# Optimization experiments

Hardware: AMD Instinct MI355X
Metric: run time of the kernel (lower is better)

The kernel has to match this reference:

```python
import jax, jax.numpy as jnp
import numpy as np

GRID = 25
NUM_NODE = GRID * GRID  # 625, hard-coded by the original module

def _neighbor_flat_indices():
    # Replicates the torch index construction exactly, incl. boundary shifts.
    offsets = np.array([[-1,-1],[-1,0],[-1,1],[0,-1],[0,0],[0,1],[1,-1],[1,0],[1,1]])
    idx = np.arange(NUM_NODE)
    rows = idx // GRID
    cols = idx % GRID
    nr = rows[:, None] + offsets[:, 0]   # [625, 9]
    nc = cols[:, None] + offsets[:, 1]
    nr = nr.reshape(GRID, GRID, 9)
    nr[0, :, :] += 1                     # reflect top boundary
    nr[-1, :, :] -= 1                    # reflect bottom boundary
    nr = nr.reshape(NUM_NODE, 9)
    nc = nc.reshape(GRID, GRID, 9)
    nc[:, 0, :] += 1                     # reflect left boundary
    nc[:, -1, :] -= 1                    # reflect right boundary
    nc = nc.reshape(NUM_NODE, 9)
    return jnp.asarray(nr * GRID + nc)   # [625, 9] flat node indices

NEIGH = _neighbor_flat_indices()

def setup_inputs() -> dict:
    key = jax.random.key(0)
    k1, k2, k3, k4, k5 = jax.random.split(key, 5)
    B = 512
    x = jax.random.normal(k1, (B, NUM_NODE, 66), dtype=jnp.float32)
    # nn.Linear(66, 64): weight [64, 66], bias [64]
    W_fc = jax.random.normal(k2, (64, 66), dtype=jnp.float32) * (1.0 / np.sqrt(66))
    b_fc = jax.random.normal(k3, (64,), dtype=jnp.float32) * 0.01
    # nn.Linear(128, 1): weight [1, 128], bias [1]
    W_at = jax.random.normal(k4, (1, 128), dtype=jnp.float32) * (1.0 / np.sqrt(128))
    b_at = jax.random.normal(k5, (1,), dtype=jnp.float32) * 0.01
    return {"x": x, "W_fc": W_fc, "b_fc": b_fc, "W_at": W_at, "b_at": b_at}

def reference(x, W_fc, b_fc, W_at, b_at):
    # h = fc(x): [B, 625, 64]
    h = jnp.einsum('bnf,df->bnd', x, W_fc) + b_fc
    # Gather fixed 9-neighbor features: [B, 625, 9, 64]
    x2 = h[:, NEIGH, :]
    # Center feature broadcast to the 9 neighbor slots: [B, 625, 9, 64]
    x1 = jnp.broadcast_to(h[:, :, None, :], x2.shape)
    z = jnp.concatenate([x1, x2], axis=-1)                  # [B, 625, 9, 128]
    s = jnp.einsum('bnkf,of->bnko', z, W_at) + b_at          # [B, 625, 9, 1]
    s = jax.nn.leaky_relu(s, negative_slope=0.01)[..., 0]    # [B, 625, 9]
    # exp(s) / sum(exp(s)) over the 9 neighbors == softmax(s)
    attn_weight = jax.nn.softmax(s, axis=-1)                 # [B, 625, 9]
    # Original: sum_k h[:, :, None, :] * w[..., None] over k
    # = h * sum_k w  (h does not depend on k); avoids a [B,625,9,64] temp.
    attn_vector = h * jnp.sum(attn_weight, axis=-1, keepdims=True)  # [B, 625, 64]
    return (attn_vector, attn_weight)
```

## Files before the change

### kernel.cpp

```cpp
#include <hip/hip_runtime.h>

#define BATCH 512
#define GRID_N 25
#define NODES 625
#define BN (BATCH * NODES)
#define NTILES (BN / 16)
#define F 66
#define D 64
#define WPB 4
#define TPW 2
#define NT_BLK (WPB * TPW)
#define STAGE_F (NT_BLK * 16 * F)
#define NBLOCKS (NTILES / NT_BLK)

typedef short bf16x8 __attribute__((ext_vector_type(8)));
typedef float f32x4  __attribute__((ext_vector_type(4)));

__device__ __forceinline__ short f2bf(float f) {
    union { float f; unsigned u; } c; c.f = f;
    unsigned r = c.u + 0x7fffu + ((c.u >> 16) & 1u);
    return (short)(r >> 16);
}

typedef const __attribute__((address_space(1))) void gas_void;
typedef __attribute__((address_space(3))) void las_void;
__device__ __forceinline__ void gload_lds16(const float* g, float* l) {
    __builtin_amdgcn_global_load_lds((gas_void*)g, (las_void*)l, 16, 0, 0);
}

__global__ __launch_bounds__(256, 3) void fc_mfma(
    const float* __restrict__ x, const float* __restrict__ Wfc,
    const float* __restrict__ bfc, const float* __restrict__ Wat,
    float* __restrict__ hout, float* __restrict__ u, float* __restrict__ v)
{
    const int tid  = threadIdx.x;
    const int lane = tid & 63;
    const int wid  = tid >> 6;
    const int l15  = lane & 15;
    const int quad = lane >> 4;

    __shared__ float stage[STAGE_F];
    __shared__ float smem[WPB * 1024];

    const size_t base = (size_t)blockIdx.x * STAGE_F;

#pragma unroll
    for (int it = 0; it < 8; ++it)
        gload_lds16(x + base + it * 1024 + tid * 4,
                    stage + it * 1024 + wid * 256);
    if (wid == 0)
        gload_lds16(x + base + 8192 + lane * 4, stage + 8192);

    bf16x8 bfrag[4][3];
#pragma unroll
    for (int t = 0; t < 4; ++t) {
        const float2* wr = (const float2*)Wfc + (t * 16 + l15) * 33;
#pragma unroll
        for (int c = 0; c < 2; ++c) {
            bf16x8 fr;
#pragma unroll
            for (int j2 = 0; j2 < 4; ++j2) {
                const float2 p = wr[c * 16 + quad * 4 + j2];
                fr[j2 * 2]     = f2bf(p.x);
                fr[j2 * 2 + 1] = f2bf(p.y);
            }
            bfrag[t][c] = fr;
        }
        bf16x8 z = {0, 0, 0, 0, 0, 0, 0, 0};
        if (quad == 0) {
            const float2 p = wr[32];
            z[0] = f2bf(p.x); z[1] = f2bf(p.y);
        }
        bfrag[t][2] = z;
    }
    float bft[4], wa1[4], wa2[4];
#pragma unroll
    for (int t = 0; t < 4; ++t) {
        bft[t] = bfc[t * 16 + l15];
        wa1[t] = Wat[t * 16 + l15];
        wa2[t] = Wat[64 + t * 16 + l15];
    }

    __syncthreads();

    float* tbuf = smem + wid * 1024;

#pragma unroll
    for (int t = 0; t < TPW; ++t) {
        const int bn0 = (blockIdx.x * NT_BLK + wid * TPW + t) * 16;

        const int node = (wid * TPW + t) * 16 + l15;
        const float2* rp = (const float2*)stage + node * 33 + quad * 4;
        bf16x8 afrag[3];
#pragma unroll
        for (int c = 0; c < 2; ++c) {
            bf16x8 fr;
#pragma unroll
            for (int j2 = 0; j2 < 4; ++j2) {
                const float2 p = rp[c * 16 + j2];
                fr[j2 * 2]     = f2bf(p.x);
                fr[j2 * 2 + 1] = f2bf(p.y);
            }
            afrag[c] = fr;
        }
        {
            bf16x8 z = {0, 0, 0, 0, 0, 0, 0, 0};
            if (quad == 0) {
                const float2 p = ((const float2*)stage)[node * 33 + 32];
                z[0] = f2bf(p.x); z[1] = f2bf(p.y);
            }
            afrag[2] = z;
        }

        f32x4 acc[4] = {{0,0,0,0},{0,0,0,0},{0,0,0,0},{0,0,0,0}};
#pragma unroll
        for (int nt = 0; nt < 4; ++nt)
#pragma unroll
            for (int c = 0; c < 3; ++c)
                acc[nt] = __builtin_amdgcn_mfma_f32_16x16x32_bf16(afrag[c], bfrag[nt][c], acc[nt], 0, 0, 0);

        float pu[4] = {0, 0, 0, 0}, pv[4] = {0, 0, 0, 0};
#pragma unroll
        for (int nt = 0; nt < 4; ++nt) {
#pragma unroll
            for (int r = 0; r < 4; ++r) {
                const float h = acc[nt][r] + bft[nt];
                tbuf[(quad * 4 + r) * 64 + nt * 16 + l15] = h;
                pu[r] = fmaf(h, wa1[nt], pu[r]);
                pv[r] = fmaf(h, wa2[nt], pv[r]);
            }
        }
#pragma unroll
        for (int off = 8; off > 0; off >>= 1) {
#pragma unroll
            for (int r = 0; r < 4; ++r) {
                pu[r] += __shfl_xor(pu[r], off, 64);
                pv[r] += __shfl_xor(pv[r], off, 64);
            }
        }
        if (l15 == 0) {
#pragma unroll
            for (int r = 0; r < 4; ++r) {
                u[bn0 + quad * 4 + r] = pu[r];
                v[bn0 + quad * 4 + r] = pv[r];
            }
        }
        float4* dst = (float4*)(hout + (size_t)bn0 * D);
        const float4* src = (const float4*)tbuf;
#pragma unroll
        for (int i = 0; i < 4; ++i)
            dst[i * 64 + lane] = src[i * 64 + lane];
    }
}

__global__ __launch_bounds__(256) void attn_kernel(
    const float* __restrict__ u, const float* __restrict__ v,
    const float* __restrict__ bat, float* __restrict__ wout)
{
    __shared__ float sw[256 * 9];
    const int tid  = threadIdx.x;
    const int lane = tid & 63;
    const int wid  = tid >> 6;
    const int bn   = blockIdx.x * 256 + tid;

    const int b   = bn / NODES;
    const int n   = bn - b * NODES;
    const int row = n / GRID_N;
    const int col = n - row * GRID_N;
    const int r0 = row + (row == 0) - (row == GRID_N - 1);
    const int c0 = col + (col == 0) - (col == GRID_N - 1);

    const float* vb = v + b * NODES;
    const float u0 = u[bn] + bat[0];

    float s[9];
#pragma unroll
    for (int k = 0; k < 9; ++k) {
        const int nr = r0 + (k / 3) - 1;
        const int nc = c0 + (k % 3) - 1;
        const float t = u0 + vb[nr * GRID_N + nc];
        s[k] = (t >= 0.0f) ? t : 0.01f * t;
    }
    float m = s[0];
#pragma unroll
    for (int k = 1; k < 9; ++k) m = fmaxf(m, s[k]);
    float sum = 0.0f;
#pragma unroll
    for (int k = 0; k < 9; ++k) { s[k] = __expf(s[k] - m); sum += s[k]; }
    const float inv = 1.0f / sum;

    float* ws = sw + wid * 576;
#pragma unroll
    for (int k = 0; k < 9; ++k) ws[lane * 9 + k] = s[k] * inv;

    float4* dst = (float4*)(wout + (size_t)(blockIdx.x * 256 + wid * 64) * 9);
    const float4* src = (const float4*)ws;
    dst[lane]      = src[lane];
    dst[64 + lane] = src[64 + lane];
    if (lane < 16) dst[128 + lane] = src[128 + lane];
}

extern "C" void kernel_launch(void* const* d_in, const int* in_sizes, int n_in,
                              void* d_out, int out_size, void* d_ws, size_t ws_size,
                              hipStream_t stream)
{
    const float* x   = (const float*)d_in[0];
    const float* Wfc = (const float*)d_in[1];
    const float* bfc = (const float*)d_in[2];
    const float* Wat = (const float*)d_in[3];
    const float* bat = (const float*)d_in[4];

    float* hout = (float*)d_out;
    float* wout = (float*)d_out + (size_t)BN * D;
    float* u = (float*)d_ws;
    float* v = u + BN;

    fc_mfma<<<NBLOCKS, 256, 0, stream>>>(x, Wfc, bfc, Wat, hout, u, v);
    attn_kernel<<<BN / 256, 256, 0, stream>>>(u, v, bat, wout);
}
```

Measured before the change: 177.5 us.

## Make fc kernel persistent over groups with double-buffered per-wave LDS prefetch

Each block now processes five tile groups instead of one, and each wave keeps its own private LDS slice. The next group's x slice is loaded into a second buffer while the current one is computed, with vmcnt waits replacing the block-wide barrier. The LDS transpose buffer for h is dropped, so h is stored straight from MFMA registers with narrower strided writes. This trades fewer blocks, lower occupancy (launch bounds 3 to 2) and less coalesced h stores for overlap of global loads with compute and less launch and sync overhead.

```diff
diff --git a/kernel.cpp b/kernel.cpp
--- a/kernel.cpp
+++ b/kernel.cpp
@@ -9,9 +9,11 @@
 #define D 64
 #define WPB 4
 #define TPW 2
-#define NT_BLK (WPB * TPW)
-#define STAGE_F (NT_BLK * 16 * F)
-#define NBLOCKS (NTILES / NT_BLK)
+#define NT_GRP (WPB * TPW)
+#define GROUP_F (NT_GRP * 16 * F)
+#define WAVE_F (TPW * 16 * F)
+#define G_PER_BLK 5
+#define NBLOCKS_P (NTILES / (NT_GRP * G_PER_BLK))
 
 typedef short bf16x8 __attribute__((ext_vector_type(8)));
 typedef float f32x4  __attribute__((ext_vector_type(4)));
@@ -28,7 +30,7 @@
     __builtin_amdgcn_global_load_lds((gas_void*)g, (las_void*)l, 16, 0, 0);
 }
 
-__global__ __launch_bounds__(256, 3) void fc_mfma(
+__global__ __launch_bounds__(256, 2) void fc_mfma(
     const float* __restrict__ x, const float* __restrict__ Wfc,
     const float* __restrict__ bfc, const float* __restrict__ Wat,
     float* __restrict__ hout, float* __restrict__ u, float* __restrict__ v)
@@ -39,17 +41,19 @@
     const int l15  = lane & 15;
     const int quad = lane >> 4;
 
-    __shared__ float stage[STAGE_F];
-    __shared__ float smem[WPB * 1024];
-
-    const size_t base = (size_t)blockIdx.x * STAGE_F;
-
-#pragma unroll
-    for (int it = 0; it < 8; ++it)
-        gload_lds16(x + base + it * 1024 + tid * 4,
-                    stage + it * 1024 + wid * 256);
-    if (wid == 0)
-        gload_lds16(x + base + 8192 + lane * 4, stage + 8192);
+    __shared__ float stage[2][WPB][WAVE_F];
+
+    const int gbase = blockIdx.x * G_PER_BLK;
+
+    {
+        const float* src = x + (size_t)gbase * GROUP_F + wid * WAVE_F;
+        float* dst = &stage[0][wid][0];
+#pragma unroll
+        for (int r = 0; r < 8; ++r)
+            gload_lds16(src + r * 256 + lane * 4, dst + r * 256);
+        if (lane < 16)
+            gload_lds16(src + 2048 + lane * 4, dst + 2048);
+    }
 
     bf16x8 bfrag[4][3];
 #pragma unroll
@@ -81,75 +85,86 @@
         wa2[t] = Wat[64 + t * 16 + l15];
     }
 
-    __syncthreads();
-
-    float* tbuf = smem + wid * 1024;
-
-#pragma unroll
-    for (int t = 0; t < TPW; ++t) {
-        const int bn0 = (blockIdx.x * NT_BLK + wid * TPW + t) * 16;
-
-        const int node = (wid * TPW + t) * 16 + l15;
-        const float2* rp = (const float2*)stage + node * 33 + quad * 4;
-        bf16x8 afrag[3];
-#pragma unroll
-        for (int c = 0; c < 2; ++c) {
-            bf16x8 fr;
-#pragma unroll
-            for (int j2 = 0; j2 < 4; ++j2) {
-                const float2 p = rp[c * 16 + j2];
-                fr[j2 * 2]     = f2bf(p.x);
-                fr[j2 * 2 + 1] = f2bf(p.y);
-            }
-            afrag[c] = fr;
-        }
-        {
-            bf16x8 z = {0, 0, 0, 0, 0, 0, 0, 0};
-            if (quad == 0) {
-                const float2 p = ((const float2*)stage)[node * 33 + 32];
-                z[0] = f2bf(p.x); z[1] = f2bf(p.y);
-            }
-            afrag[2] = z;
-        }
-
-        f32x4 acc[4] = {{0,0,0,0},{0,0,0,0},{0,0,0,0},{0,0,0,0}};
-#pragma unroll
-        for (int nt = 0; nt < 4; ++nt)
-#pragma unroll
-            for (int c = 0; c < 3; ++c)
-                acc[nt] = __builtin_amdgcn_mfma_f32_16x16x32_bf16(afrag[c], bfrag[nt][c], acc[nt], 0, 0, 0);
-
-        float pu[4] = {0, 0, 0, 0}, pv[4] = {0, 0, 0, 0};
-#pragma unroll
-        for (int nt = 0; nt < 4; ++nt) {
-#pragma unroll
-            for (int r = 0; r < 4; ++r) {
-                const float h = acc[nt][r] + bft[nt];
-                tbuf[(quad * 4 + r) * 64 + nt * 16 + l15] = h;
-                pu[r] = fmaf(h, wa1[nt], pu[r]);
-                pv[r] = fmaf(h, wa2[nt], pv[r]);
-            }
-        }
-#pragma unroll
-        for (int off = 8; off > 0; off >>= 1) {
-#pragma unroll
-            for (int r = 0; r < 4; ++r) {
-                pu[r] += __shfl_xor(pu[r], off, 64);
-                pv[r] += __shfl_xor(pv[r], off, 64);
-            }
-        }
-        if (l15 == 0) {
-#pragma unroll
-            for (int r = 0; r < 4; ++r) {
-                u[bn0 + quad * 4 + r] = pu[r];
-                v[bn0 + quad * 4 + r] = pv[r];
-            }
-        }
-        float4* dst = (float4*)(hout + (size_t)bn0 * D);
-        const float4* src = (const float4*)tbuf;
-#pragma unroll
-        for (int i = 0; i < 4; ++i)
-            dst[i * 64 + lane] = src[i * 64 + lane];
+    for (int g = 0; g < G_PER_BLK; ++g) {
+        const int s = g & 1;
+
+        if (g + 1 < G_PER_BLK) {
+            const float* src = x + (size_t)(gbase + g + 1) * GROUP_F + wid * WAVE_F;
+            float* dst = &stage[s ^ 1][wid][0];
+#pragma unroll
+            for (int r = 0; r < 8; ++r)
+                gload_lds16(src + r * 256 + lane * 4, dst + r * 256);
+            if (lane < 16)
+                gload_lds16(src + 2048 + lane * 4, dst + 2048);
+            asm volatile("s_waitcnt vmcnt(9)" ::: "memory");
+        } else {
+            asm volatile("s_waitcnt vmcnt(0)" ::: "memory");
+        }
+        __builtin_amdgcn_sched_barrier(0);
+
+        const float2* wbase = (const float2*)&stage[s][wid][0];
+
+#pragma unroll
+        for (int t = 0; t < TPW; ++t) {
+            const int bn0 = ((gbase + g) * NT_GRP + wid * TPW + t) * 16;
+            const int ln  = t * 16 + l15;
+
+            const float2* rp = wbase + ln * 33 + quad * 4;
+            bf16x8 afrag[3];
+#pragma unroll
+            for (int c = 0; c < 2; ++c) {
+                bf16x8 fr;
+#pragma unroll
+                for (int j2 = 0; j2 < 4; ++j2) {
+                    const float2 p = rp[c * 16 + j2];
+                    fr[j2 * 2]     = f2bf(p.x);
+                    fr[j2 * 2 + 1] = f2bf(p.y);
+                }
+                afrag[c] = fr;
+            }
+            {
+                bf16x8 z = {0, 0, 0, 0, 0, 0, 0, 0};
+                if (quad == 0) {
+                    const float2 p = wbase[ln * 33 + 32];
+                    z[0] = f2bf(p.x); z[1] = f2bf(p.y);
+                }
+                afrag[2] = z;
+            }
+
+            f32x4 acc[4] = {{0,0,0,0},{0,0,0,0},{0,0,0,0},{0,0,0,0}};
+#pragma unroll
+            for (int nt = 0; nt < 4; ++nt)
+#pragma unroll
+                for (int c = 0; c < 3; ++c)
+                    acc[nt] = __builtin_amdgcn_mfma_f32_16x16x32_bf16(afrag[c], bfrag[nt][c], acc[nt], 0, 0, 0);
+
+            float pu[4] = {0, 0, 0, 0}, pv[4] = {0, 0, 0, 0};
+#pragma unroll
+            for (int nt = 0; nt < 4; ++nt) {
+#pragma unroll
+                for (int r = 0; r < 4; ++r) {
+                    const float h = acc[nt][r] + bft[nt];
+                    hout[(size_t)(bn0 + quad * 4 + r) * D + nt * 16 + l15] = h;
+                    pu[r] = fmaf(h, wa1[nt], pu[r]);
+                    pv[r] = fmaf(h, wa2[nt], pv[r]);
+                }
+            }
+#pragma unroll
+            for (int off = 8; off > 0; off >>= 1) {
+#pragma unroll
+                for (int r = 0; r < 4; ++r) {
+                    pu[r] += __shfl_xor(pu[r], off, 64);
+                    pv[r] += __shfl_xor(pv[r], off, 64);
+                }
+            }
+            if (l15 == 0) {
+#pragma unroll
+                for (int r = 0; r < 4; ++r) {
+                    u[bn0 + quad * 4 + r] = pu[r];
+                    v[bn0 + quad * 4 + r] = pv[r];
+                }
+            }
+        }
     }
 }
 
@@ -215,6 +230,6 @@
     float* u = (float*)d_ws;
     float* v = u + BN;
 
-    fc_mfma<<<NBLOCKS, 256, 0, stream>>>(x, Wfc, bfc, Wat, hout, u, v);
+    fc_mfma<<<NBLOCKS_P, 256, 0, stream>>>(x, Wfc, bfc, Wat, hout, u, v);
     attn_kernel<<<BN / 256, 256, 0, stream>>>(u, v, bat, wout);
 }
```

New measurement: 174.6 us. About the same (-1.6%).
